# Kernel tuning notes

Hardware: AMD Instinct MI355X
Metric: run time of the kernel (lower is better)

The kernel has to match this reference:

```python
import jax, jax.numpy as jnp
import numpy as np


def setup_inputs() -> dict:
    key = jax.random.key(0)
    k1, k2 = jax.random.split(key)
    B, N, M = 8, 4096, 4096
    xyz1 = jax.random.normal(k1, (B, N, 3), dtype=jnp.float32)
    xyz2 = jax.random.normal(k2, (B, M, 3), dtype=jnp.float32)
    return {"xyz1": xyz1, "xyz2": xyz2}


def reference(xyz1, xyz2):
    # Squared L2 pairwise distances via the Gram trick:
    # ||x - y||^2 = ||x||^2 + ||y||^2 - 2 <x, y>
    x2 = jnp.sum(xyz1 * xyz1, axis=-1)                      # [B, N]
    y2 = jnp.sum(xyz2 * xyz2, axis=-1)                      # [B, M]
    xy = jnp.einsum('bnd,bmd->bnm', xyz1, xyz2)             # [B, N, M]
    d2 = jnp.maximum(x2[:, :, None] + y2[:, None, :] - 2.0 * xy, 0.0)
    dist1 = jnp.min(d2, axis=2)                             # [B, N] nearest in xyz2
    dist2 = jnp.min(d2, axis=1)                             # [B, M] nearest in xyz1
    # norm == 'L2' path of ChamferDistance
    return jnp.mean(dist1) + jnp.mean(dist2)
```

## Files before the change

### kernel.cpp

```cpp
#include <hip/hip_runtime.h>

#define Bc 8
#define Nc 4096
#define Mc 4096

#define BLOCK  256
#define NPT    4
#define NT     (BLOCK*NPT)
#define MT     256
#define NCHUNK (Nc/NT)
#define MCHUNK (Mc/MT)
#define BLOCKS_PER_DIR (Bc*NCHUNK*MCHUNK)

#define WS_ELEMS (Bc*Nc + Bc*Mc)

__global__ __launch_bounds__(BLOCK) void chamfer_min_kernel(
        const float* __restrict__ X1, const float* __restrict__ X2,
        unsigned* __restrict__ W, float* __restrict__ out) {
    __shared__ float4 sp[MT];

    int bid = blockIdx.x;
    if (bid == 0 && threadIdx.x == 0) out[0] = 0.0f;

    const float* qry;
    const float* cnd;
    unsigned* dmin;
    if (bid < BLOCKS_PER_DIR) {
        qry = X1; cnd = X2; dmin = W;
    } else {
        bid -= BLOCKS_PER_DIR;
        qry = X2; cnd = X1; dmin = W + Bc*Nc;
    }

    int mc = bid % MCHUNK;
    int nc = (bid / MCHUNK) % NCHUNK;
    int b  = bid / (MCHUNK * NCHUNK);

    const float* a  = qry + (size_t)b * Nc * 3;
    const float* bp = cnd + (size_t)b * Mc * 3;
    int m0 = mc * MT, n0 = nc * NT;

    {
        int m = m0 + threadIdx.x;
        float x = bp[3*m+0], y = bp[3*m+1], z = bp[3*m+2];
        sp[threadIdx.x] = make_float4(-2.0f*x, -2.0f*y, -2.0f*z,
                                      fmaf(x, x, fmaf(y, y, z*z)));
    }
    __syncthreads();

    float ax[NPT], ay[NPT], az[NPT], mn[NPT];
    #pragma unroll
    for (int k = 0; k < NPT; ++k) {
        int n = n0 + threadIdx.x + k*BLOCK;
        ax[k] = a[3*n+0]; ay[k] = a[3*n+1]; az[k] = a[3*n+2];
        mn[k] = 3.4e38f;
    }

    #pragma unroll 4
    for (int m = 0; m < MT; m += 2) {
        float4 p = sp[m];
        float4 q = sp[m+1];
        #pragma unroll
        for (int k = 0; k < NPT; ++k) {
            float t = fmaf(ax[k], p.x, p.w);
            t = fmaf(ay[k], p.y, t);
            t = fmaf(az[k], p.z, t);
            float u = fmaf(ax[k], q.x, q.w);
            u = fmaf(ay[k], q.y, u);
            u = fmaf(az[k], q.z, u);
            mn[k] = fminf(mn[k], fminf(t, u));
        }
    }

    #pragma unroll
    for (int k = 0; k < NPT; ++k) {
        int n = n0 + threadIdx.x + k*BLOCK;
        float qa = fmaf(ax[k], ax[k], fmaf(ay[k], ay[k], az[k]*az[k]));
        float d2 = fmaxf(qa + mn[k], 0.0f);
        atomicMin(&dmin[b*Nc + n], __float_as_uint(d2));
    }
}

__global__ __launch_bounds__(256) void chamfer_reduce_kernel(
        const float4* __restrict__ W4, float* __restrict__ out) {
    __shared__ float ssum[4];
    int i = blockIdx.x * blockDim.x + threadIdx.x;
    float4 v = W4[i];
    float s = (v.x + v.y) + (v.z + v.w);
    #pragma unroll
    for (int off = 32; off > 0; off >>= 1)
        s += __shfl_down(s, off, 64);
    int lane = threadIdx.x & 63, w = threadIdx.x >> 6;
    if (lane == 0) ssum[w] = s;
    __syncthreads();
    if (threadIdx.x == 0) {
        float t = (ssum[0] + ssum[1]) + (ssum[2] + ssum[3]);
        atomicAdd(out, t * (1.0f / 32768.0f));
    }
}

extern "C" void kernel_launch(void* const* d_in, const int* in_sizes, int n_in,
                              void* d_out, int out_size, void* d_ws, size_t ws_size,
                              hipStream_t stream) {
    const float* x1 = (const float*)d_in[0];
    const float* x2 = (const float*)d_in[1];
    float* out = (float*)d_out;
    unsigned* W = (unsigned*)d_ws;

    chamfer_min_kernel<<<2 * BLOCKS_PER_DIR, BLOCK, 0, stream>>>(x1, x2, W, out);
    chamfer_reduce_kernel<<<WS_ELEMS / 4 / 256, 256, 0, stream>>>((const float4*)W, out);
}
```

Baseline: 77.16 us.

## Use packed FP32 FMA and retile so each block covers all queries

Each block now processes every query point of a batch (16 per thread) against a 128-candidate tile, where before the query dimension was split into chunks. The distance FMAs use v_pk_fma_f32 inline assembly with op_sel to evaluate two query points per instruction, aiming to halve the FMA instruction count. The grid shrinks from 1024 to 512 blocks and register pressure grows, which may lower occupancy. Inline asm also limits what the compiler can schedule, and the min operations stay scalar.

After: 86.29 us. 1.12x slower.

```diff
diff --git a/kernel.cpp b/kernel.cpp
--- a/kernel.cpp
+++ b/kernel.cpp
@@ -5,79 +5,89 @@
 #define Mc 4096
 
 #define BLOCK  256
-#define NPT    4
-#define NT     (BLOCK*NPT)
-#define MT     256
-#define NCHUNK (Nc/NT)
+#define NPT    16
+#define NQP    (NPT/2)
+#define MT     128
 #define MCHUNK (Mc/MT)
-#define BLOCKS_PER_DIR (Bc*NCHUNK*MCHUNK)
+#define BLOCKS_PER_DIR (Bc*MCHUNK)
+#define WS_ELEMS (Bc*Nc + Bc*Mc)
 
-#define WS_ELEMS (Bc*Nc + Bc*Mc)
+typedef float f32x2 __attribute__((ext_vector_type(2)));
 
 __global__ __launch_bounds__(BLOCK) void chamfer_min_kernel(
         const float* __restrict__ X1, const float* __restrict__ X2,
         unsigned* __restrict__ W, float* __restrict__ out) {
-    __shared__ float4 sp[MT];
+    __shared__ f32x2 sp[MT*2];
 
     int bid = blockIdx.x;
     if (bid == 0 && threadIdx.x == 0) out[0] = 0.0f;
 
-    const float* qry;
-    const float* cnd;
-    unsigned* dmin;
-    if (bid < BLOCKS_PER_DIR) {
-        qry = X1; cnd = X2; dmin = W;
-    } else {
-        bid -= BLOCKS_PER_DIR;
-        qry = X2; cnd = X1; dmin = W + Bc*Nc;
-    }
+    const float* qry; const float* cnd; unsigned* dmin;
+    if (bid < BLOCKS_PER_DIR) { qry = X1; cnd = X2; dmin = W; }
+    else { bid -= BLOCKS_PER_DIR; qry = X2; cnd = X1; dmin = W + Bc*Nc; }
 
     int mc = bid % MCHUNK;
-    int nc = (bid / MCHUNK) % NCHUNK;
-    int b  = bid / (MCHUNK * NCHUNK);
+    int b  = bid / MCHUNK;
 
     const float* a  = qry + (size_t)b * Nc * 3;
     const float* bp = cnd + (size_t)b * Mc * 3;
-    int m0 = mc * MT, n0 = nc * NT;
+    int m0 = mc * MT;
 
-    {
+    if (threadIdx.x < MT) {
         int m = m0 + threadIdx.x;
-        float x = bp[3*m+0], y = bp[3*m+1], z = bp[3*m+2];
-        sp[threadIdx.x] = make_float4(-2.0f*x, -2.0f*y, -2.0f*z,
-                                      fmaf(x, x, fmaf(y, y, z*z)));
+        float x = bp[3*m], y = bp[3*m+1], z = bp[3*m+2];
+        sp[2*threadIdx.x]   = (f32x2){-2.0f*x, -2.0f*y};
+        sp[2*threadIdx.x+1] = (f32x2){-2.0f*z, fmaf(x, x, fmaf(y, y, z*z))};
     }
     __syncthreads();
 
-    float ax[NPT], ay[NPT], az[NPT], mn[NPT];
+    f32x2 ax[NQP], ay[NQP], az[NQP], qa[NQP], mn[NQP];
     #pragma unroll
-    for (int k = 0; k < NPT; ++k) {
-        int n = n0 + threadIdx.x + k*BLOCK;
-        ax[k] = a[3*n+0]; ay[k] = a[3*n+1]; az[k] = a[3*n+2];
-        mn[k] = 3.4e38f;
+    for (int j = 0; j < NQP; ++j) {
+        int nl = threadIdx.x + (2*j)*BLOCK;
+        int nh = threadIdx.x + (2*j+1)*BLOCK;
+        float xl = a[3*nl], yl = a[3*nl+1], zl = a[3*nl+2];
+        float xh = a[3*nh], yh = a[3*nh+1], zh = a[3*nh+2];
+        ax[j] = (f32x2){xl, xh};
+        ay[j] = (f32x2){yl, yh};
+        az[j] = (f32x2){zl, zh};
+        qa[j] = (f32x2){fmaf(xl, xl, fmaf(yl, yl, zl*zl)),
+                        fmaf(xh, xh, fmaf(yh, yh, zh*zh))};
+        mn[j] = (f32x2){3.4e38f, 3.4e38f};
     }
 
-    #pragma unroll 4
+    #pragma unroll 2
     for (int m = 0; m < MT; m += 2) {
-        float4 p = sp[m];
-        float4 q = sp[m+1];
+        f32x2 pxy = sp[2*m],   pzw = sp[2*m+1];
+        f32x2 qxy = sp[2*m+2], qzw = sp[2*m+3];
         #pragma unroll
-        for (int k = 0; k < NPT; ++k) {
-            float t = fmaf(ax[k], p.x, p.w);
-            t = fmaf(ay[k], p.y, t);
-            t = fmaf(az[k], p.z, t);
-            float u = fmaf(ax[k], q.x, q.w);
-            u = fmaf(ay[k], q.y, u);
-            u = fmaf(az[k], q.z, u);
-            mn[k] = fminf(mn[k], fminf(t, u));
+        for (int j = 0; j < NQP; ++j) {
+            f32x2 t, u;
+            asm("v_pk_fma_f32 %0, %1, %2, %3 op_sel:[0,0,1] op_sel_hi:[1,0,1]"
+                : "=v"(t) : "v"(ax[j]), "v"(pxy), "v"(pzw));
+            asm("v_pk_fma_f32 %0, %1, %2, %0 op_sel:[0,1,0] op_sel_hi:[1,1,1]"
+                : "+v"(t) : "v"(ay[j]), "v"(pxy));
+            asm("v_pk_fma_f32 %0, %1, %2, %0 op_sel:[0,0,0] op_sel_hi:[1,0,1]"
+                : "+v"(t) : "v"(az[j]), "v"(pzw));
+            asm("v_pk_fma_f32 %0, %1, %2, %3 op_sel:[0,0,1] op_sel_hi:[1,0,1]"
+                : "=v"(u) : "v"(ax[j]), "v"(qxy), "v"(qzw));
+            asm("v_pk_fma_f32 %0, %1, %2, %0 op_sel:[0,1,0] op_sel_hi:[1,1,1]"
+                : "+v"(u) : "v"(ay[j]), "v"(qxy));
+            asm("v_pk_fma_f32 %0, %1, %2, %0 op_sel:[0,0,0] op_sel_hi:[1,0,1]"
+                : "+v"(u) : "v"(az[j]), "v"(qzw));
+            mn[j].x = fminf(mn[j].x, fminf(t.x, u.x));
+            mn[j].y = fminf(mn[j].y, fminf(t.y, u.y));
         }
     }
 
     #pragma unroll
-    for (int k = 0; k < NPT; ++k) {
-        int n = n0 + threadIdx.x + k*BLOCK;
-        float qa = fmaf(ax[k], ax[k], fmaf(ay[k], ay[k], az[k]*az[k]));
-        float d2 = fmaxf(qa + mn[k], 0.0f);
-        atomicMin(&dmin[b*Nc + n], __float_as_uint(d2));
+    for (int j = 0; j < NQP; ++j) {
+        int nl = threadIdx.x + (2*j)*BLOCK;
+        int nh = threadIdx.x + (2*j+1)*BLOCK;
+        float dl = fmaxf(qa[j].x + mn[j].x, 0.0f);
+        float dh = fmaxf(qa[j].y + mn[j].y, 0.0f);
+        atomicMin(&dmin[b*Nc + nl], __float_as_uint(dl));
+        atomicMin(&dmin[b*Nc + nh], __float_as_uint(dh));
     }
 }
 
```
